# Optimization experiments

Measured on AMD Instinct MI355X. Metric: run time of the kernel, lower is better.

## Reference

```python
import jax, jax.numpy as jnp
import numpy as np

B, N = 16, 4096
N_IN, E_OUT = 128, 128          # inpt_dim[1], outp_dim[0]
OUT_N = 128                     # outp_dim[1]
G_DIM, CTXT_DIM = 64, 64
NODE_IN = E_OUT + N_IN          # 256, pre_ln size
CTXT_IN = G_DIM + CTXT_DIM      # 128
HID_F, HID_A = 256, 128
N_HEADS = 4
HEAD_DIM = OUT_N // N_HEADS     # 32
LN_EPS = 1e-5


def _init_w(key, fan_in, fan_out):
    return jax.random.normal(key, (fan_in, fan_out), jnp.float32) / np.float32(np.sqrt(fan_in))


def setup_inputs() -> dict:
    key = jax.random.key(0)
    ks = jax.random.split(key, 10)
    nodes = jax.random.normal(ks[0], (B, N, N_IN), jnp.float32)
    pooled_edges = jax.random.normal(ks[1], (B, N, E_OUT), jnp.float32)
    # variable-length graphs: valid prefix per graph (at least half the nodes)
    lengths = jax.random.randint(ks[2], (B,), N // 2, N + 1)
    mask = jnp.arange(N)[None, :] < lengths[:, None]
    globs = jax.random.normal(ks[3], (B, G_DIM), jnp.float32)
    ctxt = jax.random.normal(ks[4], (B, CTXT_DIM), jnp.float32)
    return {
        "nodes": nodes,
        "pooled_edges": pooled_edges,
        "mask": mask,
        "globs": globs,
        "ctxt": ctxt,
        "ln_g": jnp.ones((NODE_IN,), jnp.float32),
        "ln_b": jnp.zeros((NODE_IN,), jnp.float32),
        "feat_w1": _init_w(ks[5], NODE_IN + CTXT_IN, HID_F),
        "feat_b1": jnp.zeros((HID_F,), jnp.float32),
        "feat_w2": _init_w(ks[6], HID_F, OUT_N),
        "feat_b2": jnp.zeros((OUT_N,), jnp.float32),
        "attn_w1": _init_w(ks[7], NODE_IN + CTXT_IN, HID_A),
        "attn_b1": jnp.zeros((HID_A,), jnp.float32),
        "attn_w2": _init_w(ks[8], HID_A, N_HEADS),
        "attn_b2": jnp.zeros((N_HEADS,), jnp.float32),
    }


def _mlp(x, w1, b1, w2, b2):
    # DenseNetwork: one hidden block with LeakyReLU ("lrlu"), linear output
    h = jax.nn.leaky_relu(x @ w1 + b1)
    return h @ w2 + b2


def reference(nodes, pooled_edges, mask, globs, ctxt, ln_g, ln_b,
              feat_w1, feat_b1, feat_w2, feat_b2,
              attn_w1, attn_b1, attn_w2, attn_b2):
    # nodes = cat([graph.nodes, pooled_edges]) -> pre-LayerNorm
    x = jnp.concatenate([nodes, pooled_edges], axis=-1)           # [B,N,256]
    mu = jnp.mean(x, axis=-1, keepdims=True)
    var = jnp.var(x, axis=-1, keepdims=True)
    x = (x - mu) * jax.lax.rsqrt(var + LN_EPS) * ln_g + ln_b

    # high-level context broadcast to every node
    hl = jnp.concatenate([globs, ctxt], axis=-1)                   # [B,128]
    hl = jnp.broadcast_to(hl[:, None, :], (x.shape[0], x.shape[1], hl.shape[-1]))
    xin = jnp.concatenate([x, hl], axis=-1)                        # [B,N,384]

    # attention net with -inf padding, softmax over node axis (dim=-2)
    logits = _mlp(xin, attn_w1, attn_b1, attn_w2, attn_b2)          # [B,N,H]
    logits = jnp.where(mask[..., None], logits, -jnp.inf)
    w = jax.nn.softmax(logits, axis=1) / np.float32(np.sqrt(OUT_N))
    w = jnp.where(mask[..., None], w, 0.0)

    # feature net with 0 padding + residual (same_size)
    feats = _mlp(xin, feat_w1, feat_b1, feat_w2, feat_b2)           # [B,N,128]
    feats = jnp.where(mask[..., None], feats, 0.0)
    new_nodes = feats + nodes

    # expand per-head weights across head_dim, flatten, weighted node pooling
    w_full = jnp.repeat(w, HEAD_DIM, axis=-1)                       # [B,N,128]
    pooled = jnp.sum(new_nodes * w_full, axis=1)                    # [B,128]
    return (new_nodes, pooled)
```

## Files before the change

kernel.cpp:

```cpp
#include <hip/hip_runtime.h>
#include <stdint.h>

typedef unsigned short u16;
typedef unsigned char  u8;
typedef unsigned int   u32;
typedef __attribute__((ext_vector_type(8))) short bf16x8;
typedef __attribute__((ext_vector_type(4))) float f32x4;

static __device__ __forceinline__ float bf2f(u32 u) {
    union { u32 i; float f; } x; x.i = u << 16; return x.f;
}
static __device__ __forceinline__ u16 f2bf(float f) {
    union { u32 i; float f; } x; x.f = f;
    return (u16)((x.i + 0x7fffu + ((x.i >> 16) & 1u)) >> 16);
}
static __device__ __forceinline__ u32 packbf(float a, float b) {
    return (u32)f2bf(a) | ((u32)f2bf(b) << 16);
}
static __device__ __forceinline__ float ldf(const void* p, int i, int isf32) {
    return isf32 ? ((const float*)p)[i] : bf2f(((const u16*)p)[i]);
}
static __device__ __forceinline__ bool mvalid(const void* mask, int g, int mi32) {
    return mi32 ? (((const int*)mask)[g] != 0) : (((const u8*)mask)[g] != 0);
}

#define NTOT 65536
#define SXLD 264
#define SHLD 136

__global__ __launch_bounds__(256) void k0_prep(
    const void* __restrict__ feat_w1, const void* __restrict__ attn_w1,
    const void* __restrict__ feat_b1, const void* __restrict__ attn_b1,
    const void* __restrict__ feat_w2, const void* __restrict__ attn_w2,
    const void* __restrict__ globs, const void* __restrict__ ctxt,
    const void* __restrict__ ln_g,
    u16* __restrict__ W1t, u16* __restrict__ W2t, u16* __restrict__ aw2t,
    float* __restrict__ hlc)
{
    __shared__ u16 tile[64][66];
    __shared__ float hl[128];
    const int isf32 = (((const u32*)ln_g)[0] == 0x3F800000u);
    const int bid = blockIdx.x;
    const int t = threadIdx.x;

    if (bid < 24) {
        int jt = bid >> 2, kt = bid & 3;
        int j0 = jt * 64, k0 = kt * 64;
        int jj = t & 63, kq = t >> 6;
#pragma unroll
        for (int r = 0; r < 16; r++) {
            int kk = r * 4 + kq;
            int j = j0 + jj;
            float v = (j < 256) ? ldf(feat_w1, (k0 + kk) * 256 + j, isf32)
                                : ldf(attn_w1, (k0 + kk) * 128 + (j - 256), isf32);
            tile[kk][jj] = f2bf(v);
        }
        __syncthreads();
        int kk2 = t & 63, jq = t >> 6;
#pragma unroll
        for (int r = 0; r < 16; r++) {
            int jj2 = r * 4 + jq;
            W1t[(size_t)(j0 + jj2) * 256 + k0 + kk2] = tile[kk2][jj2];
        }
    } else if (bid < 32) {
        int id2 = bid - 24;
        int ct2 = id2 >> 2, kt = id2 & 3;
        int c0 = ct2 * 64, k0 = kt * 64;
        int cc = t & 63, kq = t >> 6;
#pragma unroll
        for (int r = 0; r < 16; r++) {
            int kk = r * 4 + kq;
            tile[kk][cc] = f2bf(ldf(feat_w2, (k0 + kk) * 128 + c0 + cc, isf32));
        }
        __syncthreads();
        int kk2 = t & 63, cq = t >> 6;
#pragma unroll
        for (int r = 0; r < 16; r++) {
            int cc2 = r * 4 + cq;
            W2t[(size_t)(c0 + cc2) * 256 + k0 + kk2] = tile[kk2][cc2];
        }
    } else if (bid == 32) {
#pragma unroll
        for (int i = 0; i < 8; i++) {
            int e = i * 256 + t;
            int n = e >> 7, k = e & 127;
            aw2t[e] = (n < 4) ? f2bf(ldf(attn_w2, k * 4 + n, isf32)) : (u16)0;
        }
    } else {
        int b = bid - 33;
        if (t < 64)       hl[t] = ldf(globs, b * 64 + t, isf32);
        else if (t < 128) hl[t] = ldf(ctxt, b * 64 + (t - 64), isf32);
        __syncthreads();
        {
            float s = ldf(feat_b1, t, isf32);
            for (int c = 0; c < 128; c++)
                s += hl[c] * ldf(feat_w1, (256 + c) * 256 + t, isf32);
            hlc[b * 384 + t] = s;
        }
        if (t < 128) {
            float s = ldf(attn_b1, t, isf32);
            for (int c = 0; c < 128; c++)
                s += hl[c] * ldf(attn_w1, (256 + c) * 128 + t, isf32);
            hlc[b * 384 + 256 + t] = s;
        }
    }
}

__global__ __launch_bounds__(256) void k_mega(
    const void* __restrict__ nodes, const void* __restrict__ edges,
    const void* __restrict__ ln_g, const void* __restrict__ ln_b,
    const u16* __restrict__ W1t, const u16* __restrict__ W2t,
    const u16* __restrict__ aw2t, const float* __restrict__ hlc,
    const void* __restrict__ attn_b2, const void* __restrict__ feat_b2,
    const void* __restrict__ mask,
    float* __restrict__ logits, void* __restrict__ outp)
{
    __shared__ __align__(16) u16 sX[32 * SXLD];
    __shared__ __align__(16) u16 sH[32 * SHLD];
    __shared__ float sG[256], sBt[256];
    const int t = threadIdx.x;
    const int g0 = blockIdx.x * 32;
    const int b = g0 >> 12;
    const int isf32 = (((const u32*)ln_g)[0] == 0x3F800000u);
    const int mi32  = (((const u32*)mask)[0] == 1u);

    sG[t]  = ldf(ln_g, t, isf32);
    sBt[t] = ldf(ln_b, t, isf32);
    __syncthreads();

    {
        const int r = t >> 3, q8 = t & 7;
        u32 pk[16];
#pragma unroll
        for (int j = 0; j < 4; j++) {
            int c = q8 + j * 8;
            if (isf32) {
                const float* src = (c < 16)
                    ? ((const float*)nodes + (size_t)(g0 + r) * 128 + c * 8)
                    : ((const float*)edges + (size_t)(g0 + r) * 128 + (c - 16) * 8);
                float4 v0 = ((const float4*)src)[0];
                float4 v1 = ((const float4*)src)[1];
                pk[4 * j]     = packbf(v0.x, v0.y);
                pk[4 * j + 1] = packbf(v0.z, v0.w);
                pk[4 * j + 2] = packbf(v1.x, v1.y);
                pk[4 * j + 3] = packbf(v1.z, v1.w);
            } else {
                const u16* src = (c < 16)
                    ? ((const u16*)nodes + (size_t)(g0 + r) * 128 + c * 8)
                    : ((const u16*)edges + (size_t)(g0 + r) * 128 + (c - 16) * 8);
                uint4 v = ((const uint4*)src)[0];
                pk[4 * j] = v.x; pk[4 * j + 1] = v.y;
                pk[4 * j + 2] = v.z; pk[4 * j + 3] = v.w;
            }
        }
        float s = 0.f, q = 0.f;
#pragma unroll
        for (int i = 0; i < 16; i++) {
            float lo = bf2f(pk[i] & 0xffffu), hi = bf2f(pk[i] >> 16);
            s += lo + hi; q += lo * lo + hi * hi;
        }
        s += __shfl_xor(s, 1, 64); s += __shfl_xor(s, 2, 64); s += __shfl_xor(s, 4, 64);
        q += __shfl_xor(q, 1, 64); q += __shfl_xor(q, 2, 64); q += __shfl_xor(q, 4, 64);
        float mu = s * (1.f / 256.f);
        float var = q * (1.f / 256.f) - mu * mu;
        float rs = rsqrtf(var + 1e-5f);
#pragma unroll
        for (int j = 0; j < 4; j++) {
            int c = q8 + j * 8;
            u32 ow[4];
#pragma unroll
            for (int k2 = 0; k2 < 4; k2++) {
                int col = c * 8 + k2 * 2;
                u32 w2 = pk[4 * j + k2];
                float y0 = (bf2f(w2 & 0xffffu) - mu) * rs * sG[col]     + sBt[col];
                float y1 = (bf2f(w2 >> 16)     - mu) * rs * sG[col + 1] + sBt[col + 1];
                ow[k2] = packbf(y0, y1);
            }
            *(uint4*)&sX[r * SXLD + c * 8] = make_uint4(ow[0], ow[1], ow[2], ow[3]);
        }
    }
    __syncthreads();

    const int w = t >> 6, l = t & 63;
    const int lr = l & 15, lq = l >> 4;

    f32x4 acc2[2][2];
#pragma unroll
    for (int rt = 0; rt < 2; rt++)
#pragma unroll
        for (int ct = 0; ct < 2; ct++) acc2[rt][ct] = (f32x4){0.f, 0.f, 0.f, 0.f};

    const int order[3] = {2, 0, 1};
#pragma unroll
    for (int oi = 0; oi < 3; oi++) {
        const int nt = order[oi];
        f32x4 acc1[2][2];
#pragma unroll
        for (int rt = 0; rt < 2; rt++)
#pragma unroll
            for (int ct = 0; ct < 2; ct++) acc1[rt][ct] = (f32x4){0.f, 0.f, 0.f, 0.f};

        const u16* Wp = W1t + (size_t)(nt * 128 + w * 32 + lr) * 256;
#pragma unroll
        for (int kk = 0; kk < 8; kk++) {
            bf16x8 aF[2], bF[2];
#pragma unroll
            for (int rt = 0; rt < 2; rt++)
                aF[rt] = *(const bf16x8*)&sX[(rt * 16 + lr) * SXLD + (kk * 4 + lq) * 8];
#pragma unroll
            for (int ct = 0; ct < 2; ct++)
                bF[ct] = *(const bf16x8*)(Wp + ct * 16 * 256 + kk * 32 + lq * 8);
#pragma unroll
            for (int rt = 0; rt < 2; rt++)
#pragma unroll
                for (int ct = 0; ct < 2; ct++)
                    acc1[rt][ct] = __builtin_amdgcn_mfma_f32_16x16x32_bf16(aF[rt], bF[ct], acc1[rt][ct], 0, 0, 0);
        }

        __syncthreads();
#pragma unroll
        for (int rt = 0; rt < 2; rt++)
#pragma unroll
            for (int ct = 0; ct < 2; ct++)
#pragma unroll
                for (int reg = 0; reg < 4; reg++) {
                    int row = rt * 16 + lq * 4 + reg;
                    int col = w * 32 + ct * 16 + lr;
                    float hv = acc1[rt][ct][reg] + hlc[b * 384 + nt * 128 + col];
                    hv = (hv >= 0.f) ? hv : 0.01f * hv;
                    sH[row * SHLD + col] = f2bf(hv);
                }
        __syncthreads();

        if (nt == 2) {
            if (w < 2) {
                f32x4 accL = (f32x4){0.f, 0.f, 0.f, 0.f};
#pragma unroll
                for (int kk = 0; kk < 4; kk++) {
                    bf16x8 aF = *(const bf16x8*)&sH[(w * 16 + lr) * SHLD + (kk * 4 + lq) * 8];
                    bf16x8 bF = *(const bf16x8*)(aw2t + lr * 128 + kk * 32 + lq * 8);
                    accL = __builtin_amdgcn_mfma_f32_16x16x32_bf16(aF, bF, accL, 0, 0, 0);
                }
                if (lr < 4) {
                    float bias = ldf(attn_b2, lr, isf32);
#pragma unroll
                    for (int reg = 0; reg < 4; reg++) {
                        int row = g0 + w * 16 + lq * 4 + reg;
                        logits[(size_t)lr * NTOT + row] = accL[reg] + bias;
                    }
                }
            }
        } else {
            const u16* W2p = W2t + (size_t)(w * 32 + lr) * 256 + nt * 128;
#pragma unroll
            for (int kk = 0; kk < 4; kk++) {
                bf16x8 aF[2], bF[2];
#pragma unroll
                for (int rt = 0; rt < 2; rt++)
                    aF[rt] = *(const bf16x8*)&sH[(rt * 16 + lr) * SHLD + (kk * 4 + lq) * 8];
#pragma unroll
                for (int ct = 0; ct < 2; ct++)
                    bF[ct] = *(const bf16x8*)(W2p + ct * 16 * 256 + kk * 32 + lq * 8);
#pragma unroll
                for (int rt = 0; rt < 2; rt++)
#pragma unroll
                    for (int ct = 0; ct < 2; ct++)
                        acc2[rt][ct] = __builtin_amdgcn_mfma_f32_16x16x32_bf16(aF[rt], bF[ct], acc2[rt][ct], 0, 0, 0);
            }
        }
    }

#pragma unroll
    for (int rt = 0; rt < 2; rt++)
#pragma unroll
        for (int ct = 0; ct < 2; ct++)
#pragma unroll
            for (int reg = 0; reg < 4; reg++) {
                int row = rt * 16 + lq * 4 + reg;
                int col = w * 32 + ct * 16 + lr;
                int g = g0 + row;
                float v = acc2[rt][ct][reg] + ldf(feat_b2, col, isf32);
                v = mvalid(mask, g, mi32) ? v : 0.f;
                v += ldf(nodes, g * 128 + col, isf32);
                size_t idx = (size_t)g * 128 + col;
                if (isf32) ((float*)outp)[idx] = v;
                else       ((u16*)outp)[idx] = f2bf(v);
            }
}

__global__ __launch_bounds__(1024) void k_softmax(
    const float* __restrict__ logits, const void* __restrict__ mask,
    const void* __restrict__ ln_g,
    float* __restrict__ wbuf, float* __restrict__ pooled)
{
    __shared__ float red[32];
    const int bh = blockIdx.x;
    const int b = bh >> 2, h = bh & 3;
    const int t = threadIdx.x;
    const int mi32 = (((const u32*)mask)[0] == 1u);
    if (t < 32) pooled[bh * 32 + t] = 0.f;

    float4 lg = ((const float4*)(logits + (size_t)h * NTOT + b * 4096))[t];
    int v0, v1, v2, v3;
    if (mi32) {
        int4 m4 = ((const int4*)mask)[b * 1024 + t];
        v0 = m4.x; v1 = m4.y; v2 = m4.z; v3 = m4.w;
    } else {
        u32 mb = ((const u32*)mask)[b * 1024 + t];
        v0 = mb & 255; v1 = (mb >> 8) & 255; v2 = (mb >> 16) & 255; v3 = mb >> 24;
    }
    float mx = -1e30f;
    if (v0) mx = lg.x;
    if (v1) mx = fmaxf(mx, lg.y);
    if (v2) mx = fmaxf(mx, lg.z);
    if (v3) mx = fmaxf(mx, lg.w);
#pragma unroll
    for (int o = 1; o < 64; o <<= 1) mx = fmaxf(mx, __shfl_xor(mx, o, 64));
    if ((t & 63) == 0) red[t >> 6] = mx;
    __syncthreads();
    float m2 = red[0];
#pragma unroll
    for (int i = 1; i < 16; i++) m2 = fmaxf(m2, red[i]);
    float e0 = v0 ? expf(lg.x - m2) : 0.f;
    float e1 = v1 ? expf(lg.y - m2) : 0.f;
    float e2 = v2 ? expf(lg.z - m2) : 0.f;
    float e3 = v3 ? expf(lg.w - m2) : 0.f;
    float sv = e0 + e1 + e2 + e3;
#pragma unroll
    for (int o = 1; o < 64; o <<= 1) sv += __shfl_xor(sv, o, 64);
    __syncthreads();
    if ((t & 63) == 0) red[16 + (t >> 6)] = sv;
    __syncthreads();
    float s2 = 0.f;
#pragma unroll
    for (int i = 0; i < 16; i++) s2 += red[16 + i];
    float inv = 0.08838834764831845f / s2;
    float4 o4 = make_float4(e0 * inv, e1 * inv, e2 * inv, e3 * inv);
    ((float4*)(wbuf + (size_t)h * NTOT + b * 4096))[t] = o4;
}

__global__ __launch_bounds__(256) void k_pool(
    const void* __restrict__ outp, const float* __restrict__ wbuf,
    const void* __restrict__ ln_g, float* __restrict__ pooled)
{
    __shared__ float sWn[4][256];
    __shared__ float pacc[2][128];
    const int blk = blockIdx.x;
    const int b = blk >> 4, s = blk & 15;
    const int t = threadIdx.x;
    const int isf32 = (((const u32*)ln_g)[0] == 0x3F800000u);

#pragma unroll
    for (int h = 0; h < 4; h++)
        sWn[h][t] = wbuf[(size_t)h * NTOT + b * 4096 + s * 256 + t];
    __syncthreads();

    const int ch = t & 127, rw = t >> 7;
    const int hh = ch >> 5;
    float acc = 0.f;
    if (isf32) {
        const float* op = (const float*)outp + ((size_t)(b * 4096 + s * 256)) * 128 + ch;
        for (int i = 0; i < 128; i++) {
            int nl = i * 2 + rw;
            acc += op[(size_t)nl * 128] * sWn[hh][nl];
        }
    } else {
        const u16* op = (const u16*)outp + ((size_t)(b * 4096 + s * 256)) * 128 + ch;
        for (int i = 0; i < 128; i++) {
            int nl = i * 2 + rw;
            acc += bf2f(op[(size_t)nl * 128]) * sWn[hh][nl];
        }
    }
    pacc[rw][ch] = acc;
    __syncthreads();
    if (t < 128) atomicAdd(&pooled[b * 128 + t], pacc[0][t] + pacc[1][t]);
}

__global__ __launch_bounds__(256) void k_fin(const float* __restrict__ pooled,
                                             const void* __restrict__ ln_g,
                                             void* __restrict__ outbase)
{
    int t = blockIdx.x * 256 + threadIdx.x;
    const int isf32 = (((const u32*)ln_g)[0] == 0x3F800000u);
    if (t < 2048) {
        size_t off = (size_t)NTOT * 128 + t;
        if (isf32) ((float*)outbase)[off] = pooled[t];
        else       ((u16*)outbase)[off] = f2bf(pooled[t]);
    }
}

extern "C" void kernel_launch(void* const* d_in, const int* in_sizes, int n_in,
                              void* d_out, int out_size, void* d_ws, size_t ws_size,
                              hipStream_t stream)
{
    const void* nodes   = d_in[0];
    const void* edges   = d_in[1];
    const void* mask    = d_in[2];
    const void* globs   = d_in[3];
    const void* ctxt    = d_in[4];
    const void* ln_g    = d_in[5];
    const void* ln_b    = d_in[6];
    const void* feat_w1 = d_in[7];
    const void* feat_b1 = d_in[8];
    const void* feat_w2 = d_in[9];
    const void* feat_b2 = d_in[10];
    const void* attn_w1 = d_in[11];
    const void* attn_b1 = d_in[12];
    const void* attn_w2 = d_in[13];
    const void* attn_b2 = d_in[14];

    char* ws = (char*)d_ws;
    u16*   W1t    = (u16*)ws;   ws += (size_t)384 * 256 * 2;
    u16*   W2t    = (u16*)ws;   ws += (size_t)128 * 256 * 2;
    u16*   aw2t   = (u16*)ws;   ws += (size_t)16 * 128 * 2;
    float* hlc    = (float*)ws; ws += (size_t)16 * 384 * 4;
    float* logits = (float*)ws; ws += (size_t)NTOT * 4 * 4;
    float* wbuf   = (float*)ws; ws += (size_t)NTOT * 4 * 4;
    float* pooled = (float*)ws; ws += (size_t)2048 * 4;

    k0_prep  <<<dim3(49),   dim3(256),  0, stream>>>(feat_w1, attn_w1, feat_b1, attn_b1,
                                                     feat_w2, attn_w2, globs, ctxt, ln_g,
                                                     W1t, W2t, aw2t, hlc);
    k_mega   <<<dim3(2048), dim3(256),  0, stream>>>(nodes, edges, ln_g, ln_b, W1t, W2t,
                                                     aw2t, hlc, attn_b2, feat_b2, mask,
                                                     logits, d_out);
    k_softmax<<<dim3(64),   dim3(1024), 0, stream>>>(logits, mask, ln_g, wbuf, pooled);
    k_pool   <<<dim3(256),  dim3(256),  0, stream>>>(d_out, wbuf, ln_g, pooled);
    k_fin    <<<dim3(8),    dim3(256),  0, stream>>>(pooled, ln_g, d_out);
}
```

Before: 242.2 us.

## Double row tile in fused MLP kernel and widen pooling parallelism

```diff
diff --git a/kernel.cpp b/kernel.cpp
--- a/kernel.cpp
+++ b/kernel.cpp
@@ -27,6 +27,7 @@
 #define NTOT 65536
 #define SXLD 264
 #define SHLD 136
+#define BM   64
 
 __global__ __launch_bounds__(256) void k0_prep(
     const void* __restrict__ feat_w1, const void* __restrict__ attn_w1,
@@ -93,12 +94,14 @@
         __syncthreads();
         {
             float s = ldf(feat_b1, t, isf32);
+#pragma unroll 8
             for (int c = 0; c < 128; c++)
                 s += hl[c] * ldf(feat_w1, (256 + c) * 256 + t, isf32);
             hlc[b * 384 + t] = s;
         }
         if (t < 128) {
             float s = ldf(attn_b1, t, isf32);
+#pragma unroll 8
             for (int c = 0; c < 128; c++)
                 s += hl[c] * ldf(attn_w1, (256 + c) * 128 + t, isf32);
             hlc[b * 384 + 256 + t] = s;
@@ -106,7 +109,7 @@
     }
 }
 
-__global__ __launch_bounds__(256) void k_mega(
+__global__ __launch_bounds__(256, 3) void k_mega(
     const void* __restrict__ nodes, const void* __restrict__ edges,
     const void* __restrict__ ln_g, const void* __restrict__ ln_b,
     const u16* __restrict__ W1t, const u16* __restrict__ W2t,
@@ -115,11 +118,11 @@
     const void* __restrict__ mask,
     float* __restrict__ logits, void* __restrict__ outp)
 {
-    __shared__ __align__(16) u16 sX[32 * SXLD];
-    __shared__ __align__(16) u16 sH[32 * SHLD];
+    __shared__ __align__(16) u16 sX[BM * SXLD];
+    __shared__ __align__(16) u16 sH[BM * SHLD];
     __shared__ float sG[256], sBt[256];
     const int t = threadIdx.x;
-    const int g0 = blockIdx.x * 32;
+    const int g0 = blockIdx.x * BM;
     const int b = g0 >> 12;
     const int isf32 = (((const u32*)ln_g)[0] == 0x3F800000u);
     const int mi32  = (((const u32*)mask)[0] == 1u);
@@ -128,8 +131,9 @@
     sBt[t] = ldf(ln_b, t, isf32);
     __syncthreads();
 
-    {
-        const int r = t >> 3, q8 = t & 7;
+#pragma unroll
+    for (int half = 0; half < 2; half++) {
+        const int r = half * 32 + (t >> 3), q8 = t & 7;
         u32 pk[16];
 #pragma unroll
         for (int j = 0; j < 4; j++) {
@@ -184,9 +188,9 @@
     const int w = t >> 6, l = t & 63;
     const int lr = l & 15, lq = l >> 4;
 
-    f32x4 acc2[2][2];
-#pragma unroll
-    for (int rt = 0; rt < 2; rt++)
+    f32x4 acc2[4][2];
+#pragma unroll
+    for (int rt = 0; rt < 4; rt++)
 #pragma unroll
         for (int ct = 0; ct < 2; ct++) acc2[rt][ct] = (f32x4){0.f, 0.f, 0.f, 0.f};
 
@@ -194,84 +198,97 @@
 #pragma unroll
     for (int oi = 0; oi < 3; oi++) {
         const int nt = order[oi];
-        f32x4 acc1[2][2];
-#pragma unroll
-        for (int rt = 0; rt < 2; rt++)
+
+        float hbv[2];
+#pragma unroll
+        for (int ct = 0; ct < 2; ct++)
+            hbv[ct] = hlc[b * 384 + nt * 128 + w * 32 + ct * 16 + lr];
+
+        f32x4 acc1[4][2];
+#pragma unroll
+        for (int rt = 0; rt < 4; rt++)
 #pragma unroll
             for (int ct = 0; ct < 2; ct++) acc1[rt][ct] = (f32x4){0.f, 0.f, 0.f, 0.f};
 
         const u16* Wp = W1t + (size_t)(nt * 128 + w * 32 + lr) * 256;
 #pragma unroll
-        for (int kk = 0; kk < 8; kk++) {
-            bf16x8 aF[2], bF[2];
-#pragma unroll
-            for (int rt = 0; rt < 2; rt++)
-                aF[rt] = *(const bf16x8*)&sX[(rt * 16 + lr) * SXLD + (kk * 4 + lq) * 8];
-#pragma unroll
-            for (int ct = 0; ct < 2; ct++)
-                bF[ct] = *(const bf16x8*)(Wp + ct * 16 * 256 + kk * 32 + lq * 8);
-#pragma unroll
-            for (int rt = 0; rt < 2; rt++)
+        for (int kh = 0; kh < 2; kh++) {
+            bf16x8 bW[4][2];
+#pragma unroll
+            for (int kk = 0; kk < 4; kk++)
 #pragma unroll
                 for (int ct = 0; ct < 2; ct++)
-                    acc1[rt][ct] = __builtin_amdgcn_mfma_f32_16x16x32_bf16(aF[rt], bF[ct], acc1[rt][ct], 0, 0, 0);
+                    bW[kk][ct] = *(const bf16x8*)(Wp + ct * 16 * 256 + (kh * 4 + kk) * 32 + lq * 8);
+#pragma unroll
+            for (int kk = 0; kk < 4; kk++) {
+                bf16x8 aF[4];
+#pragma unroll
+                for (int rt = 0; rt < 4; rt++)
+                    aF[rt] = *(const bf16x8*)&sX[(rt * 16 + lr) * SXLD + ((kh * 4 + kk) * 4 + lq) * 8];
+#pragma unroll
+                for (int rt = 0; rt < 4; rt++)
+#pragma unroll
+                    for (int ct = 0; ct < 2; ct++)
+                        acc1[rt][ct] = __builtin_amdgcn_mfma_f32_16x16x32_bf16(aF[rt], bW[kk][ct], acc1[rt][ct], 0, 0, 0);
+            }
         }
 
         __syncthreads();
 #pragma unroll
-        for (int rt = 0; rt < 2; rt++)
+        for (int rt = 0; rt < 4; rt++)
 #pragma unroll
             for (int ct = 0; ct < 2; ct++)
 #pragma unroll
                 for (int reg = 0; reg < 4; reg++) {
                     int row = rt * 16 + lq * 4 + reg;
                     int col = w * 32 + ct * 16 + lr;
-                    float hv = acc1[rt][ct][reg] + hlc[b * 384 + nt * 128 + col];
+                    float hv = acc1[rt][ct][reg] + hbv[ct];
                     hv = (hv >= 0.f) ? hv : 0.01f * hv;
                     sH[row * SHLD + col] = f2bf(hv);
                 }
         __syncthreads();
 
         if (nt == 2) {
-            if (w < 2) {
-                f32x4 accL = (f32x4){0.f, 0.f, 0.f, 0.f};
-#pragma unroll
-                for (int kk = 0; kk < 4; kk++) {
-                    bf16x8 aF = *(const bf16x8*)&sH[(w * 16 + lr) * SHLD + (kk * 4 + lq) * 8];
-                    bf16x8 bF = *(const bf16x8*)(aw2t + lr * 128 + kk * 32 + lq * 8);
-                    accL = __builtin_amdgcn_mfma_f32_16x16x32_bf16(aF, bF, accL, 0, 0, 0);
-                }
-                if (lr < 4) {
-                    float bias = ldf(attn_b2, lr, isf32);
-#pragma unroll
-                    for (int reg = 0; reg < 4; reg++) {
-                        int row = g0 + w * 16 + lq * 4 + reg;
-                        logits[(size_t)lr * NTOT + row] = accL[reg] + bias;
-                    }
+            f32x4 accL = (f32x4){0.f, 0.f, 0.f, 0.f};
+#pragma unroll
+            for (int kk = 0; kk < 4; kk++) {
+                bf16x8 aF = *(const bf16x8*)&sH[(w * 16 + lr) * SHLD + (kk * 4 + lq) * 8];
+                bf16x8 bF = *(const bf16x8*)(aw2t + lr * 128 + kk * 32 + lq * 8);
+                accL = __builtin_amdgcn_mfma_f32_16x16x32_bf16(aF, bF, accL, 0, 0, 0);
+            }
+            if (lr < 4) {
+                float bias = ldf(attn_b2, lr, isf32);
+#pragma unroll
+                for (int reg = 0; reg < 4; reg++) {
+                    int row = g0 + w * 16 + lq * 4 + reg;
+                    logits[(size_t)lr * NTOT + row] = accL[reg] + bias;
                 }
             }
         } else {
             const u16* W2p = W2t + (size_t)(w * 32 + lr) * 256 + nt * 128;
+            bf16x8 bW2[4][2];
+#pragma unroll
+            for (int kk = 0; kk < 4; kk++)
+#pragma unroll
+                for (int ct = 0; ct < 2; ct++)
+                    bW2[kk][ct] = *(const bf16x8*)(W2p + ct * 16 * 256 + kk * 32 + lq * 8);
 #pragma unroll
             for (int kk = 0; kk < 4; kk++) {
-                bf16x8 aF[2], bF[2];
-#pragma unroll
-                for (int rt = 0; rt < 2; rt++)
+                bf16x8 aF[4];
+#pragma unroll
+                for (int rt = 0; rt < 4; rt++)
                     aF[rt] = *(const bf16x8*)&sH[(rt * 16 + lr) * SHLD + (kk * 4 + lq) * 8];
 #pragma unroll
-                for (int ct = 0; ct < 2; ct++)
-                    bF[ct] = *(const bf16x8*)(W2p + ct * 16 * 256 + kk * 32 + lq * 8);
-#pragma unroll
-                for (int rt = 0; rt < 2; rt++)
+                for (int rt = 0; rt < 4; rt++)
 #pragma unroll
                     for (int ct = 0; ct < 2; ct++)
-                        acc2[rt][ct] = __builtin_amdgcn_mfma_f32_16x16x32_bf16(aF[rt], bF[ct], acc2[rt][ct], 0, 0, 0);
-            }
-        }
-    }
-
-#pragma unroll
-    for (int rt = 0; rt < 2; rt++)
+                        acc2[rt][ct] = __builtin_amdgcn_mfma_f32_16x16x32_bf16(aF[rt], bW2[kk][ct], acc2[rt][ct], 0, 0, 0);
+            }
+        }
+    }
+
+#pragma unroll
+    for (int rt = 0; rt < 4; rt++)
 #pragma unroll
         for (int ct = 0; ct < 2; ct++)
 #pragma unroll
@@ -343,37 +360,51 @@
     const void* __restrict__ outp, const float* __restrict__ wbuf,
     const void* __restrict__ ln_g, float* __restrict__ pooled)
 {
-    __shared__ float sWn[4][256];
-    __shared__ float pacc[2][128];
+    __shared__ float sW[4][32];
+    __shared__ float pacc[8][128];
     const int blk = blockIdx.x;
-    const int b = blk >> 4, s = blk & 15;
+    const int b = blk >> 7, s = blk & 127;
     const int t = threadIdx.x;
     const int isf32 = (((const u32*)ln_g)[0] == 0x3F800000u);
 
-#pragma unroll
-    for (int h = 0; h < 4; h++)
-        sWn[h][t] = wbuf[(size_t)h * NTOT + b * 4096 + s * 256 + t];
-    __syncthreads();
-
-    const int ch = t & 127, rw = t >> 7;
-    const int hh = ch >> 5;
-    float acc = 0.f;
+    if (t < 128) {
+        int h = t >> 5, n = t & 31;
+        sW[h][n] = wbuf[(size_t)h * NTOT + b * 4096 + s * 32 + n];
+    }
+    __syncthreads();
+
+    const int c4 = (t & 31) * 4, r8 = t >> 5;
+    const int h = c4 >> 5;
+    const size_t rowbase = (size_t)(b * 4096 + s * 32);
+    float a0 = 0.f, a1 = 0.f, a2 = 0.f, a3 = 0.f;
     if (isf32) {
-        const float* op = (const float*)outp + ((size_t)(b * 4096 + s * 256)) * 128 + ch;
-        for (int i = 0; i < 128; i++) {
-            int nl = i * 2 + rw;
-            acc += op[(size_t)nl * 128] * sWn[hh][nl];
+        const float* op = (const float*)outp;
+#pragma unroll
+        for (int i = 0; i < 4; i++) {
+            int row = i * 8 + r8;
+            float4 v = *(const float4*)(op + (rowbase + row) * 128 + c4);
+            float wv = sW[h][row];
+            a0 += v.x * wv; a1 += v.y * wv; a2 += v.z * wv; a3 += v.w * wv;
         }
     } else {
-        const u16* op = (const u16*)outp + ((size_t)(b * 4096 + s * 256)) * 128 + ch;
-        for (int i = 0; i < 128; i++) {
-            int nl = i * 2 + rw;
-            acc += bf2f(op[(size_t)nl * 128]) * sWn[hh][nl];
-        }
-    }
-    pacc[rw][ch] = acc;
-    __syncthreads();
-    if (t < 128) atomicAdd(&pooled[b * 128 + t], pacc[0][t] + pacc[1][t]);
+        const u16* op = (const u16*)outp;
+#pragma unroll
+        for (int i = 0; i < 4; i++) {
+            int row = i * 8 + r8;
+            uint2 v = *(const uint2*)(op + (rowbase + row) * 128 + c4);
+            float wv = sW[h][row];
+            a0 += bf2f(v.x & 0xffffu) * wv; a1 += bf2f(v.x >> 16) * wv;
+            a2 += bf2f(v.y & 0xffffu) * wv; a3 += bf2f(v.y >> 16) * wv;
+        }
+    }
+    *(float4*)&pacc[r8][c4] = make_float4(a0, a1, a2, a3);
+    __syncthreads();
+    if (t < 128) {
+        float sum = 0.f;
+#pragma unroll
+        for (int r = 0; r < 8; r++) sum += pacc[r][t];
+        atomicAdd(&pooled[b * 128 + t], sum);
+    }
 }
 
 __global__ __launch_bounds__(256) void k_fin(const float* __restrict__ pooled,
@@ -421,10 +452,10 @@
     k0_prep  <<<dim3(49),   dim3(256),  0, stream>>>(feat_w1, attn_w1, feat_b1, attn_b1,
                                                      feat_w2, attn_w2, globs, ctxt, ln_g,
                                                      W1t, W2t, aw2t, hlc);
-    k_mega   <<<dim3(2048), dim3(256),  0, stream>>>(nodes, edges, ln_g, ln_b, W1t, W2t,
+    k_mega   <<<dim3(1024), dim3(256),  0, stream>>>(nodes, edges, ln_g, ln_b, W1t, W2t,
                                                      aw2t, hlc, attn_b2, feat_b2, mask,
                                                      logits, d_out);
     k_softmax<<<dim3(64),   dim3(1024), 0, stream>>>(logits, mask, ln_g, wbuf, pooled);
-    k_pool   <<<dim3(256),  dim3(256),  0, stream>>>(d_out, wbuf, ln_g, pooled);
+    k_pool   <<<dim3(2048), dim3(256),  0, stream>>>(d_out, wbuf, ln_g, pooled);
     k_fin    <<<dim3(8),    dim3(256),  0, stream>>>(pooled, ln_g, d_out);
 }
```

New measurement: 229.0 us. 5.5% less time.
